# Kernel tuning notes

Measured on AMD Instinct MI355X. Metric: run time of the kernel, lower is better.

## Reference

```python
import jax, jax.numpy as jnp
import numpy as np

N = 100000   # nodes
E = 3200000  # edges
CY = 128     # channels_y (signal length per node)
HID = 10     # hidden_channels
H = 2        # heads
C = 10       # out channels per head
BN_EPS = 1e-5


def _glorot(k, shape):
    lim = float(np.sqrt(6.0 / (shape[0] + shape[1])))
    return jax.random.uniform(k, shape, jnp.float32, -lim, lim)


def setup_inputs() -> dict:
    key = jax.random.key(0)
    ks = jax.random.split(key, 16)
    p = {}
    p["signal"] = jax.random.normal(ks[0], (N, CY), jnp.float32)
    p["edge_index"] = jax.random.randint(ks[1], (2, E), 0, N)
    p["edge_weight"] = jax.random.uniform(ks[2], (E,), jnp.float32)
    p["mask"] = jax.random.bernoulli(ks[3], 0.3, (N,))
    # mlp_in: Linear(CY,512) -> BatchNorm -> ReLU -> Linear(512,HID) (PyG MLP, plain_last)
    p["W1"] = _glorot(ks[4], (CY, 512)); p["b1"] = jnp.zeros((512,), jnp.float32)
    p["gamma"] = jnp.ones((512,), jnp.float32); p["beta"] = jnp.zeros((512,), jnp.float32)
    p["W2"] = _glorot(ks[5], (512, HID)); p["b2"] = jnp.zeros((HID,), jnp.float32)
    # GATv2Conv(HID, HID, heads=2, edge_dim=1, concat=True)
    p["Wl"] = _glorot(ks[6], (HID, H * C)); p["bl"] = jnp.zeros((H * C,), jnp.float32)
    p["Wr"] = _glorot(ks[7], (HID, H * C)); p["br"] = jnp.zeros((H * C,), jnp.float32)
    p["We"] = _glorot(ks[8], (1, H * C))              # lin_edge, no bias
    p["att"] = _glorot(ks[9], (H, C))                 # attention vector per head
    p["gat_bias"] = jnp.zeros((H * C,), jnp.float32)
    # mlp_out: MLP([20,512]) single layer, plain_last -> just Linear (dropout off in eval)
    p["W3"] = _glorot(ks[10], (H * C, 512)); p["b3"] = jnp.zeros((512,), jnp.float32)
    # out_linear: Linear(512, CY)
    p["W4"] = _glorot(ks[11], (512, CY)); p["b4"] = jnp.zeros((CY,), jnp.float32)
    return p


def _forward(signal, edge_index, edge_weight, mask,
             W1, b1, gamma, beta, W2, b2,
             Wl, bl, Wr, br, We, att, gat_bias,
             W3, b3, W4, b4):
    # node masking: (signal.T * ~mask).T
    x = signal * (~mask)[:, None].astype(signal.dtype)
    # mlp_in (eval mode: BN with running mean=0, var=1)
    x = x @ W1 + b1
    x = x * (gamma / jnp.sqrt(jnp.asarray(1.0 + BN_EPS, x.dtype))) + beta
    x = jax.nn.relu(x)
    x = x @ W2 + b2                                   # [N, HID]
    # GATv2Conv
    src, dst = edge_index[0], edge_index[1]
    xl = (x @ Wl + bl).reshape(N, H, C)               # source transform
    xr = (x @ Wr + br).reshape(N, H, C)               # target transform
    ea = (edge_weight[:, None] @ We).reshape(E, H, C)  # edge feature transform
    e = jax.nn.leaky_relu(xl[src] + xr[dst] + ea, 0.2)  # [E,H,C]
    alpha = jnp.einsum('ehc,hc->eh', e, att)          # [E,H]
    # segment softmax over incoming edges of each dst node
    m = jax.ops.segment_max(alpha, dst, num_segments=N)
    ex = jnp.exp(alpha - m[dst])
    den = jax.ops.segment_sum(ex, dst, num_segments=N)
    a = ex / (den[dst] + 1e-16)                       # [E,H]
    out = jax.ops.segment_sum(xl[src] * a[:, :, None], dst, num_segments=N)
    out = out.reshape(N, H * C) + gat_bias            # concat heads + bias
    # mlp_out (single plain-last layer) + out_linear
    out = out @ W3 + b3
    out = out @ W4 + b4
    return out


def reference(signal, edge_index, edge_weight, mask,
              W1, b1, gamma, beta, W2, b2,
              Wl, bl, Wr, br, We, att, gat_bias,
              W3, b3, W4, b4):
    return _forward(signal, edge_index, edge_weight, mask,
                    W1, b1, gamma, beta, W2, b2,
                    Wl, bl, Wr, br, We, att, gat_bias,
                    W3, b3, W4, b4)
```

## Files before the change

kernel.cpp:

```cpp
#include <hip/hip_runtime.h>
#include <hip/hip_bf16.h>

constexpr int NN = 100000;
constexpr int NE = 3200000;
constexpr int CYC = 128;
constexpr int NB = 1563;
constexpr int EBLK = 256;
constexpr int ECHUNK = NE / EBLK;
constexpr int MSCAN = NB * EBLK;
constexpr int CAP = 2432;

#define OFF_W1T    0u
#define OFF_W2T    131072u
#define OFF_B1E    147456u
#define OFF_SMALL  149504u
#define OFF_W34    151808u
#define OFF_B34    162048u
#define OFF_FLAGS  162560u
#define OFF_XLB    163840u
#define OFF_XR     6563840u
#define OFF_GH     14563840u
#define OFF_BB     16164352u
#define OFF_BS     16170752u
#define OFF_BIN    16171776u

#define SF_WLR 0
#define SF_BLR 400
#define SF_ATT 440
#define SF_WE  460
#define SF_GB  480
#define SF_B2  500

typedef __attribute__((ext_vector_type(8))) short bf16x8;
typedef __attribute__((ext_vector_type(4))) float f32x4;

__device__ __forceinline__ float bfu(unsigned short x) {
  return __uint_as_float(((unsigned)x) << 16);
}
__device__ __forceinline__ short f2bf(float f) {
  __hip_bfloat16 h = __float2bfloat16(f);
  return *reinterpret_cast<short*>(&h);
}
__device__ __forceinline__ float LD(const void* p, long i, int f32f) {
  return f32f ? ((const float*)p)[i] : bfu(((const unsigned short*)p)[i]);
}

__global__ __launch_bounds__(256) void kPrep(
    const void* __restrict__ W1, const void* __restrict__ b1,
    const void* __restrict__ gamma, const void* __restrict__ beta,
    const void* __restrict__ W2, const void* __restrict__ b2,
    const void* __restrict__ Wl, const void* __restrict__ bl,
    const void* __restrict__ Wr, const void* __restrict__ br,
    const void* __restrict__ We, const void* __restrict__ att,
    const void* __restrict__ gbias, const void* __restrict__ W3,
    const void* __restrict__ b3, const void* __restrict__ W4,
    const void* __restrict__ b4, const void* __restrict__ mask,
    int* __restrict__ flags,
    short* __restrict__ W1T, float* __restrict__ b1eff, short* __restrict__ W2T,
    float* __restrict__ smallf, float* __restrict__ W34, float* __restrict__ b34)
{
  __shared__ int sfl[2];
  int t = threadIdx.x;
  if (t < 64) {
    const unsigned short* W1u = (const unsigned short*)W1;
    const unsigned* masku = (const unsigned*)mask;
    int big = 0;
#pragma unroll
    for (int k = 0; k < 8; k++) {
      unsigned e = (W1u[t * 8 + k] >> 7) & 0xFF;
      if (e >= 170) big++;
    }
    int byt = 0;
#pragma unroll
    for (int k = 0; k < 4; k++) if (masku[t * 4 + k] & ~1u) byt = 1;
#pragma unroll
    for (int o = 1; o < 64; o <<= 1) {
      big += __shfl_xor(big, o);
      byt |= __shfl_xor(byt, o);
    }
    if (t == 0) {
      sfl[0] = (big >= 4) ? 1 : 0;
      sfl[1] = byt;
      if (blockIdx.x == 0) { flags[0] = sfl[0]; flags[1] = byt; }
    }
  }
  __syncthreads();
  const int f32f = sfl[0];

  int tid = blockIdx.x * 256 + t;
  const float rs = 0.999995000037f;
  if (tid < 65536) {
    int j = tid >> 7, k = tid & 127;
    float s = LD(gamma, j, f32f) * rs;
    W1T[j * 128 + k] = f2bf(LD(W1, k * 512 + j, f32f) * s);
    if (k == 0) b1eff[j] = LD(b1, j, f32f) * s + LD(beta, j, f32f);
  } else if (tid < 73728) {
    int i = tid - 65536;
    int c = i >> 9, k = i & 511;
    W2T[c * 512 + k] = (c < 10) ? f2bf(LD(W2, k * 10 + c, f32f)) : (short)0;
  } else if (tid < 76288) {
    int i = tid - 73728;
    int j = i >> 7, tt = i & 127;
    float acc = 0.f;
    for (int k = 0; k < 512; k++) acc += LD(W3, j * 512 + k, f32f) * LD(W4, k * 128 + tt, f32f);
    W34[j * 128 + tt] = acc;
  } else if (tid < 76416) {
    int tt = tid - 76288;
    float acc = LD(b4, tt, f32f);
    for (int k = 0; k < 512; k++) acc += LD(b3, k, f32f) * LD(W4, k * 128 + tt, f32f);
    b34[tt] = acc;
  } else if (tid < 76932) {
    int i = tid - 76416;
    if (i < 400) {
      int c = i / 40, o = i % 40;
      smallf[SF_WLR + i] = (o < 20) ? LD(Wl, c * 20 + o, f32f) : LD(Wr, c * 20 + (o - 20), f32f);
    } else if (i < 440) {
      int o = i - 400;
      smallf[SF_BLR + o] = (o < 20) ? LD(bl, o, f32f) : LD(br, o - 20, f32f);
    } else if (i < 460) {
      smallf[SF_ATT + (i - 440)] = LD(att, i - 440, f32f);
    } else if (i < 480) {
      smallf[SF_WE + (i - 460)] = LD(We, i - 460, f32f);
    } else if (i < 500) {
      smallf[SF_GB + (i - 480)] = LD(gbias, i - 480, f32f);
    } else {
      int c = i - 500;
      smallf[SF_B2 + c] = (c < 10) ? LD(b2, c, f32f) : 0.f;
    }
  }
}

__global__ __launch_bounds__(256, 3) void kA(
    const void* __restrict__ sig, const void* __restrict__ mask,
    const short* __restrict__ W1T, const float* __restrict__ b1eff,
    const short* __restrict__ W2T, const float* __restrict__ smallf,
    const int* __restrict__ flags,
    unsigned short* __restrict__ xlb, float* __restrict__ xr)
{
  __shared__ short h1[32][520];
  __shared__ float xhp[4][32][16];
  __shared__ float xh[32][12];
  __shared__ float sWlr[400];
  __shared__ float sblr[40];
  __shared__ float sb1[512];
  __shared__ float sb2[16];

  const int f32f = flags[0];
  const int mk8  = flags[1];
  int t = threadIdx.x;
  for (int i = t; i < 512; i += 256) sb1[i] = b1eff[i];
  for (int i = t; i < 400; i += 256) sWlr[i] = smallf[SF_WLR + i];
  if (t < 40) sblr[t] = smallf[SF_BLR + t];
  if (t < 16) sb2[t] = smallf[SF_B2 + t];

  int w = t >> 6, l = t & 63;
  int lrow = l & 15, quad = l >> 4;
  int row0 = blockIdx.x * 32;

  bf16x8 zz = {0, 0, 0, 0, 0, 0, 0, 0};
  bf16x8 af[2][4];
#pragma unroll
  for (int rt = 0; rt < 2; rt++) {
    int arow = row0 + rt * 16 + lrow;
    bool mbit = mk8 ? (((const unsigned char*)mask)[arow] != 0)
                    : (((const int*)mask)[arow] != 0);
    if (mbit) {
#pragma unroll
      for (int kt = 0; kt < 4; kt++) af[rt][kt] = zz;
    } else if (f32f) {
      const float4* Sf = (const float4*)((const float*)sig + (size_t)arow * CYC);
#pragma unroll
      for (int kt = 0; kt < 4; kt++) {
        float4 x0 = Sf[kt * 8 + quad * 2];
        float4 x1 = Sf[kt * 8 + quad * 2 + 1];
        bf16x8 v;
        v[0] = f2bf(x0.x); v[1] = f2bf(x0.y); v[2] = f2bf(x0.z); v[3] = f2bf(x0.w);
        v[4] = f2bf(x1.x); v[5] = f2bf(x1.y); v[6] = f2bf(x1.z); v[7] = f2bf(x1.w);
        af[rt][kt] = v;
      }
    } else {
      const bf16x8* Ap = (const bf16x8*)((const unsigned short*)sig + (size_t)arow * CYC);
#pragma unroll
      for (int kt = 0; kt < 4; kt++) af[rt][kt] = Ap[kt * 4 + quad];
    }
  }

  f32x4 acc[2][8];
#pragma unroll
  for (int rt = 0; rt < 2; rt++)
#pragma unroll
    for (int ct = 0; ct < 8; ct++) acc[rt][ct] = (f32x4){0.f, 0.f, 0.f, 0.f};
  const bf16x8* Bp = (const bf16x8*)W1T;
#pragma unroll
  for (int kt = 0; kt < 4; kt++) {
#pragma unroll
    for (int ct = 0; ct < 8; ct++) {
      bf16x8 bv = Bp[(w * 128 + ct * 16 + lrow) * 16 + kt * 4 + quad];
      acc[0][ct] = __builtin_amdgcn_mfma_f32_16x16x32_bf16(af[0][kt], bv, acc[0][ct], 0, 0, 0);
      acc[1][ct] = __builtin_amdgcn_mfma_f32_16x16x32_bf16(af[1][kt], bv, acc[1][ct], 0, 0, 0);
    }
  }
  __syncthreads();
#pragma unroll
  for (int rt = 0; rt < 2; rt++)
#pragma unroll
    for (int ct = 0; ct < 8; ct++) {
      int col = w * 128 + ct * 16 + lrow;
      float bb = sb1[col];
#pragma unroll
      for (int r = 0; r < 4; r++) {
        float v = fmaxf(acc[rt][ct][r] + bb, 0.f);
        h1[rt * 16 + quad * 4 + r][col] = f2bf(v);
      }
    }
  __syncthreads();

  f32x4 a2acc[2];
  a2acc[0] = (f32x4){0.f, 0.f, 0.f, 0.f};
  a2acc[1] = (f32x4){0.f, 0.f, 0.f, 0.f};
  const bf16x8* B2p = (const bf16x8*)W2T;
#pragma unroll
  for (int kt2 = 0; kt2 < 4; kt2++) {
    bf16x8 b2v = B2p[lrow * 64 + w * 16 + kt2 * 4 + quad];
    bf16x8 a20 = *(const bf16x8*)&h1[lrow][w * 128 + kt2 * 32 + quad * 8];
    bf16x8 a21 = *(const bf16x8*)&h1[16 + lrow][w * 128 + kt2 * 32 + quad * 8];
    a2acc[0] = __builtin_amdgcn_mfma_f32_16x16x32_bf16(a20, b2v, a2acc[0], 0, 0, 0);
    a2acc[1] = __builtin_amdgcn_mfma_f32_16x16x32_bf16(a21, b2v, a2acc[1], 0, 0, 0);
  }
#pragma unroll
  for (int rt = 0; rt < 2; rt++)
#pragma unroll
    for (int r = 0; r < 4; r++) xhp[w][rt * 16 + quad * 4 + r][lrow] = a2acc[rt][r];
  __syncthreads();

  for (int i = t; i < 320; i += 256) {
    int row = i / 10, c = i % 10;
    xh[row][c] = xhp[0][row][c] + xhp[1][row][c] + xhp[2][row][c] + xhp[3][row][c] + sb2[c];
  }
  __syncthreads();

  for (int i = t; i < 1280; i += 256) {
    int row = i & 31, o = i >> 5;
    float v = sblr[o];
#pragma unroll
    for (int c = 0; c < 10; c++) v += xh[row][c] * sWlr[c * 40 + o];
    int gr = row0 + row;
    if (o < 10)      xlb[(size_t)gr * 32 + o] = (unsigned short)f2bf(v);
    else if (o < 20) xlb[(size_t)gr * 32 + 6 + o] = (unsigned short)f2bf(v);
    else             xr[(size_t)gr * 20 + (o - 20)] = v;
  }
}

__global__ __launch_bounds__(256) void kB1(const int* __restrict__ ei,
                                           int* __restrict__ gh) {
  __shared__ int h[NB];
  int t = threadIdx.x, blk = blockIdx.x;
  for (int i = t; i < NB; i += 256) h[i] = 0;
  __syncthreads();
  const int* dst = ei + NE;
  int base = blk * ECHUNK, bend = base + ECHUNK;
  for (int i = base + t; i < bend; i += 256)
    atomicAdd(&h[dst[i] >> 6], 1);
  __syncthreads();
  for (int i = t; i < NB; i += 256) gh[i * EBLK + blk] = h[i];
}

__global__ __launch_bounds__(256) void kS1(const int* __restrict__ gh,
                                           int* __restrict__ ghx,
                                           int* __restrict__ bsum) {
  __shared__ int sS[256];
  int t = threadIdx.x;
  int base = blockIdx.x * 2048 + t * 8;
  int d[8], tsum = 0;
#pragma unroll
  for (int k = 0; k < 8; k++) {
    d[k] = (base + k < MSCAN) ? gh[base + k] : 0;
    tsum += d[k];
  }
  sS[t] = tsum;
  __syncthreads();
  for (int o = 1; o < 256; o <<= 1) {
    int v = (t >= o) ? sS[t - o] : 0;
    __syncthreads();
    sS[t] += v;
    __syncthreads();
  }
  int run = sS[t] - tsum;
#pragma unroll
  for (int k = 0; k < 8; k++) {
    if (base + k < MSCAN) ghx[base + k] = run;
    run += d[k];
  }
  if (t == 255) bsum[blockIdx.x] = sS[255];
}

__global__ __launch_bounds__(256) void kS2(int* __restrict__ bsum, int nb) {
  __shared__ int sS[256];
  int t = threadIdx.x;
  int v = (t < nb) ? bsum[t] : 0;
  sS[t] = v;
  __syncthreads();
  for (int o = 1; o < 256; o <<= 1) {
    int u = (t >= o) ? sS[t - o] : 0;
    __syncthreads();
    sS[t] += u;
    __syncthreads();
  }
  if (t < nb) bsum[t] = sS[t] - v;
}

__global__ __launch_bounds__(256) void kS3(int* __restrict__ gh,
                                           const int* __restrict__ bsum,
                                           int* __restrict__ bb) {
  int i = blockIdx.x * 256 + threadIdx.x;
  int v = gh[i] + bsum[i >> 11];
  gh[i] = v;
  if ((i & 255) == 0) bb[i >> 8] = v;
  if (i == 0) bb[NB] = NE;
}

__global__ __launch_bounds__(256) void kB3(const int* __restrict__ ei,
                                           const void* __restrict__ ew,
                                           const int* __restrict__ flags,
                                           const int* __restrict__ gh,
                                           int2* __restrict__ binned) {
  __shared__ int cur[NB];
  const int f32f = flags[0];
  int t = threadIdx.x, blk = blockIdx.x;
  for (int i = t; i < NB; i += 256) cur[i] = gh[i * EBLK + blk];
  __syncthreads();
  int base = blk * ECHUNK, bend = base + ECHUNK;
  for (int i = base + t; i < bend; i += 256) {
    int s = ei[i], d = ei[NE + i];
    float w = LD(ew, i, f32f);
    int b = d >> 6;
    int pos = atomicAdd(&cur[b], 1);
    binned[pos] = make_int2(s | ((d & 63) << 17), __float_as_int(w));
  }
}

__global__ __launch_bounds__(256) void kSrtAgg(
    const int* __restrict__ bb, const int2* __restrict__ binned,
    const unsigned short* __restrict__ xlb, const float* __restrict__ xr,
    const float* __restrict__ smallf, const float* __restrict__ W34,
    const float* __restrict__ b34, const int* __restrict__ flags,
    void* __restrict__ out)
{
  __shared__ int2  sES[CAP];
  __shared__ float sXr[64 * 20];
  __shared__ float sW[2560];
  __shared__ int   sCnt[64];
  __shared__ int   sPre[64];
  __shared__ int   sStart[64];
  __shared__ int   sCur[64];
  __shared__ float sb[128];
  __shared__ float sAtt[20], sWe[20], sGb[20];

  const int f32f = flags[0];
  int t = threadIdx.x, b = blockIdx.x;
  int node0 = b * 64;

  for (int i = t; i < 2560; i += 256) sW[i] = W34[i];
  for (int i = t; i < 1280; i += 256) {
    int gi = node0 * 20 + i;
    sXr[i] = (gi < NN * 20) ? xr[gi] : 0.f;
  }
  if (t < 128) sb[t] = b34[t];
  if (t < 64) sCnt[t] = 0;
  if (t < 20) { sAtt[t] = smallf[SF_ATT + t]; sWe[t] = smallf[SF_WE + t]; sGb[t] = smallf[SF_GB + t]; }
  __syncthreads();

  int base = bb[b], end = bb[b + 1];
  int ne = end - base;

  for (int i = t; i < ne; i += 256)
    atomicAdd(&sCnt[(unsigned)binned[base + i].x >> 17], 1);
  __syncthreads();

  if (t < 64) sPre[t] = sCnt[t];
  __syncthreads();
  for (int o = 1; o < 64; o <<= 1) {
    int v = 0;
    if (t < 64 && t >= o) v = sPre[t - o];
    __syncthreads();
    if (t < 64) sPre[t] += v;
    __syncthreads();
  }
  if (t < 64) {
    int ex = sPre[t] - sCnt[t];
    sStart[t] = ex;
    sCur[t] = ex;
  }
  __syncthreads();

  for (int i = t; i < ne; i += 256) {
    int2 e = binned[base + i];
    int dl = (unsigned)e.x >> 17;
    int pos = atomicAdd(&sCur[dl], 1);
    if (pos < CAP) sES[pos] = make_int2(e.x & 0x1FFFF, e.y);
  }
  __syncthreads();

  int n = t >> 2, head = (t >> 1) & 1, part = t & 1;
  float xrw[10], attw[10], wew[10];
#pragma unroll
  for (int c = 0; c < 10; c++) {
    xrw[c]  = sXr[n * 20 + head * 10 + c];
    attw[c] = sAtt[head * 10 + c];
    wew[c]  = sWe[head * 10 + c];
  }
  float acc[10];
#pragma unroll
  for (int c = 0; c < 10; c++) acc[c] = 0.f;
  float den = 0.f;
  int s0 = sStart[n];
  int s1 = s0 + sCnt[n];
  if (s1 > CAP) s1 = CAP;
  for (int i = s0 + part; i < s1; i += 2) {
    int2 e = sES[i];
    const unsigned short* p = xlb + (size_t)e.x * 32 + head * 16;
    uint4 q = *(const uint4*)p;
    unsigned q4 = *(const unsigned*)(p + 8);
    float vl[10];
    unsigned qq[5] = {q.x, q.y, q.z, q.w, q4};
#pragma unroll
    for (int k = 0; k < 5; k++) {
      vl[2 * k]     = __uint_as_float(qq[k] << 16);
      vl[2 * k + 1] = __uint_as_float(qq[k] & 0xffff0000u);
    }
    float ww = __int_as_float(e.y);
    float a = 0.f;
#pragma unroll
    for (int c = 0; c < 10; c++) {
      float v = vl[c] + xrw[c] + ww * wew[c];
      v = fmaxf(v, 0.2f * v);
      a += v * attw[c];
    }
    float pp = __expf(a);
    den += pp;
#pragma unroll
    for (int c = 0; c < 10; c++) acc[c] += pp * vl[c];
  }
  den += __shfl_xor(den, 1);
#pragma unroll
  for (int c = 0; c < 10; c++) acc[c] += __shfl_xor(acc[c], 1);

  __syncthreads();
  if (part == 0) {
    float inv = 1.f / (den + 1e-16f);
#pragma unroll
    for (int c = 0; c < 10; c++)
      sXr[n * 20 + head * 10 + c] = acc[c] * inv + sGb[head * 10 + c];
  }
  __syncthreads();

  int col = t & 127, half = t >> 7;
  for (int n2 = half; n2 < 64; n2 += 2) {
    int gn = node0 + n2;
    if (gn >= NN) break;
    float v = sb[col];
    const float* g = &sXr[n2 * 20];
#pragma unroll
    for (int c = 0; c < 20; c++) v += g[c] * sW[c * 128 + col];
    if (f32f) ((float*)out)[(size_t)gn * 128 + col] = v;
    else ((unsigned short*)out)[(size_t)gn * 128 + col] = (unsigned short)f2bf(v);
  }
}

extern "C" void kernel_launch(void* const* d_in, const int* in_sizes, int n_in,
                              void* d_out, int out_size, void* d_ws, size_t ws_size,
                              hipStream_t stream) {
  (void)in_sizes; (void)n_in; (void)out_size; (void)ws_size;
  const void* sig  = d_in[0];
  const int*  ei   = (const int*)d_in[1];
  const void* ew   = d_in[2];
  const void* mask = d_in[3];
  const void* W1   = d_in[4];
  const void* b1   = d_in[5];
  const void* gam  = d_in[6];
  const void* bet  = d_in[7];
  const void* W2   = d_in[8];
  const void* b2   = d_in[9];
  const void* Wl   = d_in[10];
  const void* bl   = d_in[11];
  const void* Wr   = d_in[12];
  const void* br   = d_in[13];
  const void* We   = d_in[14];
  const void* att  = d_in[15];
  const void* gb   = d_in[16];
  const void* W3   = d_in[17];
  const void* b3   = d_in[18];
  const void* W4   = d_in[19];
  const void* b4   = d_in[20];

  char* ws = (char*)d_ws;
  short* W1T    = (short*)(ws + OFF_W1T);
  short* W2T    = (short*)(ws + OFF_W2T);
  float* b1eff  = (float*)(ws + OFF_B1E);
  float* smallf = (float*)(ws + OFF_SMALL);
  float* W34    = (float*)(ws + OFF_W34);
  float* b34    = (float*)(ws + OFF_B34);
  int*   flags  = (int*)(ws + OFF_FLAGS);
  unsigned short* xlb = (unsigned short*)(ws + OFF_XLB);
  float* xr     = (float*)(ws + OFF_XR);
  int*   gh     = (int*)(ws + OFF_GH);
  int*   bb     = (int*)(ws + OFF_BB);
  int*   bsum   = (int*)(ws + OFF_BS);
  int2*  bincsr = (int2*)(ws + OFF_BIN);

  kPrep<<<301, 256, 0, stream>>>(W1, b1, gam, bet, W2, b2, Wl, bl, Wr, br, We, att,
                                 gb, W3, b3, W4, b4, mask, flags,
                                 W1T, b1eff, W2T, smallf, W34, b34);
  kA<<<NN / 32, 256, 0, stream>>>(sig, mask, W1T, b1eff, W2T, smallf, flags, xlb, xr);
  kB1<<<EBLK, 256, 0, stream>>>(ei, gh);
  kS1<<<(MSCAN + 2047) / 2048, 256, 0, stream>>>(gh, gh, bsum);
  kS2<<<1, 256, 0, stream>>>(bsum, (MSCAN + 2047) / 2048);
  kS3<<<NB, 256, 0, stream>>>(gh, bsum, bb);
  kB3<<<EBLK, 256, 0, stream>>>(ei, ew, flags, gh, bincsr);
  kSrtAgg<<<NB, 256, 0, stream>>>(bb, bincsr, xlb, xr, smallf, W34, b34, flags, d_out);
}
```

Measured before the change: 471.4 us.

## Retile node MLP kernel to 64 rows with staged LDS input and coalesced stores

The node MLP kernel now processes 64 rows per block instead of 32, so each W1 fragment loaded from global memory feeds four MFMA row tiles rather than two. The signal tile is first loaded coalesced into LDS, the hidden activations go through per-wave LDS buffers in two halves, and the final xl/xr outputs are staged in LDS and written with packed, coalesced stores. The cost is higher register and LDS use, with occupancy lowered from 3 to 2 blocks per SM, plus added tail handling because 100000 is not a multiple of 64. This kernel is only one stage of the pipeline, so its effect on total time is limited.

```diff
diff --git a/kernel.cpp b/kernel.cpp
--- a/kernel.cpp
+++ b/kernel.cpp
@@ -9,6 +9,7 @@
 constexpr int ECHUNK = NE / EBLK;
 constexpr int MSCAN = NB * EBLK;
 constexpr int CAP = 2432;
+constexpr int NBLK_A = (NN + 63) / 64;
 
 #define OFF_W1T    0u
 #define OFF_W2T    131072u
@@ -130,124 +131,166 @@
   }
 }
 
-__global__ __launch_bounds__(256, 3) void kA(
+__global__ __launch_bounds__(256, 2) void kA(
     const void* __restrict__ sig, const void* __restrict__ mask,
     const short* __restrict__ W1T, const float* __restrict__ b1eff,
     const short* __restrict__ W2T, const float* __restrict__ smallf,
     const int* __restrict__ flags,
     unsigned short* __restrict__ xlb, float* __restrict__ xr)
 {
-  __shared__ short h1[32][520];
-  __shared__ float xhp[4][32][16];
-  __shared__ float xh[32][12];
+  __shared__ __align__(16) char sR1[17408];
+  __shared__ short sH[4][32 * 136];
+  __shared__ float sb1[512];
+  __shared__ float sxh[64][12];
   __shared__ float sWlr[400];
   __shared__ float sblr[40];
-  __shared__ float sb1[512];
   __shared__ float sb2[16];
+
+  short (*sA)[136]        = (short (*)[136])sR1;
+  float (*sxhp)[64][17]   = (float (*)[64][17])sR1;
+  float (*sxlr)[40]       = (float (*)[40])sR1;
 
   const int f32f = flags[0];
   const int mk8  = flags[1];
   int t = threadIdx.x;
+  int w = t >> 6, l = t & 63;
+  int lrow = l & 15, quad = l >> 4;
+  int row0 = blockIdx.x * 64;
+
   for (int i = t; i < 512; i += 256) sb1[i] = b1eff[i];
   for (int i = t; i < 400; i += 256) sWlr[i] = smallf[SF_WLR + i];
   if (t < 40) sblr[t] = smallf[SF_BLR + t];
   if (t < 16) sb2[t] = smallf[SF_B2 + t];
 
-  int w = t >> 6, l = t & 63;
-  int lrow = l & 15, quad = l >> 4;
-  int row0 = blockIdx.x * 32;
-
   bf16x8 zz = {0, 0, 0, 0, 0, 0, 0, 0};
-  bf16x8 af[2][4];
-#pragma unroll
-  for (int rt = 0; rt < 2; rt++) {
-    int arow = row0 + rt * 16 + lrow;
-    bool mbit = mk8 ? (((const unsigned char*)mask)[arow] != 0)
-                    : (((const int*)mask)[arow] != 0);
+#pragma unroll
+  for (int k = 0; k < 4; k++) {
+    int idx = t + k * 256;
+    int row = idx >> 4, seg = idx & 15;
+    int gr = row0 + row;
+    int grc = gr < NN ? gr : NN - 1;
+    bool mbit = mk8 ? (((const unsigned char*)mask)[grc] != 0)
+                    : (((const int*)mask)[grc] != 0);
+    bf16x8 v;
     if (mbit) {
-#pragma unroll
-      for (int kt = 0; kt < 4; kt++) af[rt][kt] = zz;
+      v = zz;
     } else if (f32f) {
-      const float4* Sf = (const float4*)((const float*)sig + (size_t)arow * CYC);
-#pragma unroll
-      for (int kt = 0; kt < 4; kt++) {
-        float4 x0 = Sf[kt * 8 + quad * 2];
-        float4 x1 = Sf[kt * 8 + quad * 2 + 1];
-        bf16x8 v;
-        v[0] = f2bf(x0.x); v[1] = f2bf(x0.y); v[2] = f2bf(x0.z); v[3] = f2bf(x0.w);
-        v[4] = f2bf(x1.x); v[5] = f2bf(x1.y); v[6] = f2bf(x1.z); v[7] = f2bf(x1.w);
-        af[rt][kt] = v;
+      const float4* Sf = (const float4*)((const float*)sig + (size_t)grc * CYC) + seg * 2;
+      float4 x0 = Sf[0], x1 = Sf[1];
+      v[0] = f2bf(x0.x); v[1] = f2bf(x0.y); v[2] = f2bf(x0.z); v[3] = f2bf(x0.w);
+      v[4] = f2bf(x1.x); v[5] = f2bf(x1.y); v[6] = f2bf(x1.z); v[7] = f2bf(x1.w);
+    } else {
+      v = ((const bf16x8*)((const unsigned short*)sig + (size_t)grc * CYC))[seg];
+    }
+    *(bf16x8*)&sA[row][seg * 8] = v;
+  }
+  __syncthreads();
+
+  float bcol[8];
+#pragma unroll
+  for (int ct = 0; ct < 8; ct++) bcol[ct] = sb1[w * 128 + ct * 16 + lrow];
+
+  f32x4 acc[4][8];
+#pragma unroll
+  for (int rf = 0; rf < 4; rf++)
+#pragma unroll
+    for (int ct = 0; ct < 8; ct++) acc[rf][ct] = (f32x4){0.f, 0.f, 0.f, 0.f};
+
+  const bf16x8* Bp = (const bf16x8*)W1T;
+  int bvbase = w * 2048 + lrow * 16 + quad;
+#pragma unroll
+  for (int kt = 0; kt < 4; kt++) {
+    bf16x8 a0 = *(const bf16x8*)&sA[lrow][kt * 32 + quad * 8];
+    bf16x8 a1 = *(const bf16x8*)&sA[16 + lrow][kt * 32 + quad * 8];
+    bf16x8 a2f = *(const bf16x8*)&sA[32 + lrow][kt * 32 + quad * 8];
+    bf16x8 a3 = *(const bf16x8*)&sA[48 + lrow][kt * 32 + quad * 8];
+#pragma unroll
+    for (int ct = 0; ct < 8; ct++) {
+      bf16x8 bv = Bp[bvbase + ct * 256 + kt * 4];
+      acc[0][ct] = __builtin_amdgcn_mfma_f32_16x16x32_bf16(a0, bv, acc[0][ct], 0, 0, 0);
+      acc[1][ct] = __builtin_amdgcn_mfma_f32_16x16x32_bf16(a1, bv, acc[1][ct], 0, 0, 0);
+      acc[2][ct] = __builtin_amdgcn_mfma_f32_16x16x32_bf16(a2f, bv, acc[2][ct], 0, 0, 0);
+      acc[3][ct] = __builtin_amdgcn_mfma_f32_16x16x32_bf16(a3, bv, acc[3][ct], 0, 0, 0);
+    }
+  }
+  __syncthreads();
+
+  const bf16x8* B2p = (const bf16x8*)W2T;
+  bf16x8 b2v[4];
+#pragma unroll
+  for (int kt2 = 0; kt2 < 4; kt2++) b2v[kt2] = B2p[lrow * 64 + w * 16 + kt2 * 4 + quad];
+
+  short* hb = &sH[w][0];
+#pragma unroll
+  for (int hf = 0; hf < 2; hf++) {
+#pragma unroll
+    for (int rr = 0; rr < 2; rr++) {
+      int rf = hf * 2 + rr;
+#pragma unroll
+      for (int ct = 0; ct < 8; ct++) {
+        float bb = bcol[ct];
+#pragma unroll
+        for (int r = 0; r < 4; r++) {
+          float vv = fmaxf(acc[rf][ct][r] + bb, 0.f);
+          hb[(rr * 16 + quad * 4 + r) * 136 + ct * 16 + lrow] = f2bf(vv);
+        }
       }
-    } else {
-      const bf16x8* Ap = (const bf16x8*)((const unsigned short*)sig + (size_t)arow * CYC);
-#pragma unroll
-      for (int kt = 0; kt < 4; kt++) af[rt][kt] = Ap[kt * 4 + quad];
-    }
-  }
-
-  f32x4 acc[2][8];
-#pragma unroll
-  for (int rt = 0; rt < 2; rt++)
-#pragma unroll
-    for (int ct = 0; ct < 8; ct++) acc[rt][ct] = (f32x4){0.f, 0.f, 0.f, 0.f};
-  const bf16x8* Bp = (const bf16x8*)W1T;
-#pragma unroll
-  for (int kt = 0; kt < 4; kt++) {
-#pragma unroll
-    for (int ct = 0; ct < 8; ct++) {
-      bf16x8 bv = Bp[(w * 128 + ct * 16 + lrow) * 16 + kt * 4 + quad];
-      acc[0][ct] = __builtin_amdgcn_mfma_f32_16x16x32_bf16(af[0][kt], bv, acc[0][ct], 0, 0, 0);
-      acc[1][ct] = __builtin_amdgcn_mfma_f32_16x16x32_bf16(af[1][kt], bv, acc[1][ct], 0, 0, 0);
-    }
-  }
-  __syncthreads();
-#pragma unroll
-  for (int rt = 0; rt < 2; rt++)
-#pragma unroll
-    for (int ct = 0; ct < 8; ct++) {
-      int col = w * 128 + ct * 16 + lrow;
-      float bb = sb1[col];
-#pragma unroll
-      for (int r = 0; r < 4; r++) {
-        float v = fmaxf(acc[rt][ct][r] + bb, 0.f);
-        h1[rt * 16 + quad * 4 + r][col] = f2bf(v);
-      }
-    }
-  __syncthreads();
-
-  f32x4 a2acc[2];
-  a2acc[0] = (f32x4){0.f, 0.f, 0.f, 0.f};
-  a2acc[1] = (f32x4){0.f, 0.f, 0.f, 0.f};
-  const bf16x8* B2p = (const bf16x8*)W2T;
-#pragma unroll
-  for (int kt2 = 0; kt2 < 4; kt2++) {
-    bf16x8 b2v = B2p[lrow * 64 + w * 16 + kt2 * 4 + quad];
-    bf16x8 a20 = *(const bf16x8*)&h1[lrow][w * 128 + kt2 * 32 + quad * 8];
-    bf16x8 a21 = *(const bf16x8*)&h1[16 + lrow][w * 128 + kt2 * 32 + quad * 8];
-    a2acc[0] = __builtin_amdgcn_mfma_f32_16x16x32_bf16(a20, b2v, a2acc[0], 0, 0, 0);
-    a2acc[1] = __builtin_amdgcn_mfma_f32_16x16x32_bf16(a21, b2v, a2acc[1], 0, 0, 0);
-  }
-#pragma unroll
-  for (int rt = 0; rt < 2; rt++)
-#pragma unroll
-    for (int r = 0; r < 4; r++) xhp[w][rt * 16 + quad * 4 + r][lrow] = a2acc[rt][r];
-  __syncthreads();
-
-  for (int i = t; i < 320; i += 256) {
-    int row = i / 10, c = i % 10;
-    xh[row][c] = xhp[0][row][c] + xhp[1][row][c] + xhp[2][row][c] + xhp[3][row][c] + sb2[c];
-  }
-  __syncthreads();
-
-  for (int i = t; i < 1280; i += 256) {
-    int row = i & 31, o = i >> 5;
+    }
+    asm volatile("s_waitcnt lgkmcnt(0)" ::: "memory");
+
+    f32x4 a2[2];
+    a2[0] = (f32x4){0.f, 0.f, 0.f, 0.f};
+    a2[1] = (f32x4){0.f, 0.f, 0.f, 0.f};
+#pragma unroll
+    for (int kt2 = 0; kt2 < 4; kt2++) {
+      bf16x8 x0 = *(const bf16x8*)&hb[lrow * 136 + kt2 * 32 + quad * 8];
+      bf16x8 x1 = *(const bf16x8*)&hb[(16 + lrow) * 136 + kt2 * 32 + quad * 8];
+      a2[0] = __builtin_amdgcn_mfma_f32_16x16x32_bf16(x0, b2v[kt2], a2[0], 0, 0, 0);
+      a2[1] = __builtin_amdgcn_mfma_f32_16x16x32_bf16(x1, b2v[kt2], a2[1], 0, 0, 0);
+    }
+#pragma unroll
+    for (int f = 0; f < 2; f++)
+#pragma unroll
+      for (int r = 0; r < 4; r++)
+        sxhp[w][hf * 32 + f * 16 + quad * 4 + r][lrow] = a2[f][r];
+  }
+  __syncthreads();
+
+  for (int i = t; i < 640; i += 256) {
+    int row = i / 10, c = i - row * 10;
+    sxh[row][c] = sxhp[0][row][c] + sxhp[1][row][c] + sxhp[2][row][c] + sxhp[3][row][c] + sb2[c];
+  }
+  __syncthreads();
+
+  for (int i = t; i < 2560; i += 256) {
+    int row = i / 40, o = i - row * 40;
     float v = sblr[o];
 #pragma unroll
-    for (int c = 0; c < 10; c++) v += xh[row][c] * sWlr[c * 40 + o];
-    int gr = row0 + row;
-    if (o < 10)      xlb[(size_t)gr * 32 + o] = (unsigned short)f2bf(v);
-    else if (o < 20) xlb[(size_t)gr * 32 + 6 + o] = (unsigned short)f2bf(v);
-    else             xr[(size_t)gr * 20 + (o - 20)] = v;
+    for (int c = 0; c < 10; c++) v += sxh[row][c] * sWlr[c * 40 + o];
+    sxlr[row][o] = v;
+  }
+  __syncthreads();
+
+  int nrows = NN - row0; if (nrows > 64) nrows = 64;
+  unsigned* xlb32 = (unsigned*)xlb;
+#pragma unroll
+  for (int k = 0; k < 4; k++) {
+    int i = t + k * 256;
+    int row = i >> 4, p = i & 15;
+    if (row < nrows) {
+      int s0 = 2 * p, s1 = 2 * p + 1;
+      float lo = (s0 < 10) ? sxlr[row][s0] : (s0 >= 16 && s0 < 26) ? sxlr[row][s0 - 6] : 0.f;
+      float hi = (s1 < 10) ? sxlr[row][s1] : (s1 >= 16 && s1 < 26) ? sxlr[row][s1 - 6] : 0.f;
+      unsigned u = (unsigned)(unsigned short)f2bf(lo) |
+                   ((unsigned)(unsigned short)f2bf(hi) << 16);
+      xlb32[(size_t)(row0 + row) * 16 + p] = u;
+    }
+  }
+#pragma unroll
+  for (int k = 0; k < 5; k++) {
+    int i = t + k * 256;
+    int row = i / 20, c = i - row * 20;
+    if (row < nrows) xr[(size_t)(row0 + row) * 20 + c] = sxlr[row][20 + c];
   }
 }
 
@@ -511,7 +554,7 @@
   kPrep<<<301, 256, 0, stream>>>(W1, b1, gam, bet, W2, b2, Wl, bl, Wr, br, We, att,
                                  gb, W3, b3, W4, b4, mask, flags,
                                  W1T, b1eff, W2T, smallf, W34, b34);
-  kA<<<NN / 32, 256, 0, stream>>>(sig, mask, W1T, b1eff, W2T, smallf, flags, xlb, xr);
+  kA<<<NBLK_A, 256, 0, stream>>>(sig, mask, W1T, b1eff, W2T, smallf, flags, xlb, xr);
   kB1<<<EBLK, 256, 0, stream>>>(ei, gh);
   kS1<<<(MSCAN + 2047) / 2048, 256, 0, stream>>>(gh, gh, bsum);
   kS2<<<1, 256, 0, stream>>>(bsum, (MSCAN + 2047) / 2048);
```

After: 448.0 us. -5.0%, faster.
